# Performance work log

Measured on AMD Instinct MI355X. Metric: run time of the kernel, lower is better.

Reference implementation:

```python
import jax, jax.numpy as jnp
import numpy as np

OUT_DIM = 4096
IN_DIM = 4096
N_NNZ = 1600000
BATCH = 8192


def setup_inputs() -> dict:
    key = jax.random.key(0)
    k1, k2, k3 = jax.random.split(key, 3)
    x = jax.random.normal(k1, (BATCH, IN_DIM), dtype=jnp.float32)
    # COO indices of the transposed kernel: (row=output idx, col=input idx)
    rows = jax.random.randint(k2, (N_NNZ, 1), 0, OUT_DIM, dtype=jnp.int64)
    cols = jax.random.randint(jax.random.fold_in(k2, 1), (N_NNZ, 1), 0, IN_DIM, dtype=jnp.int64)
    indices = jnp.concatenate([rows, cols], axis=1)  # (N_NNZ, 2)
    values = jax.random.normal(k3, (N_NNZ,), dtype=jnp.float32) * 0.02
    return {"x": x, "indices": indices, "values": values}


def reference(x, indices, values):
    # kernel_t is a sparse (OUT_DIM, IN_DIM) matrix. In JAX the efficient
    # faithful form is to scatter the nonzeros into a dense matrix (duplicate
    # indices sum, matching SpMM semantics) and do a single dense GEMM.
    rows = indices[:, 0]
    cols = indices[:, 1]
    W_t = jnp.zeros((OUT_DIM, IN_DIM), dtype=values.dtype).at[rows, cols].add(values)
    # output = (kernel_t @ x^T)^T = x @ kernel_t^T, then ReLU activation.
    out = jax.nn.relu(jnp.einsum("bi,oi->bo", x, W_t))
    return out
```

## Files before the change

### kernel.cpp

```cpp
#include <hip/hip_runtime.h>
#include <hip/hip_bf16.h>
#include <stdint.h>

#define M_DIM 8192
#define N_DIM 4096
#define K_DIM 4096
#define NNZ   1600000

typedef __attribute__((ext_vector_type(8))) short bf16x8;
typedef __attribute__((ext_vector_type(4))) float f32x4;

static const size_t WF32_OFF  = 0;
static const size_t WBF16_OFF = 64ull << 20;
static const size_t XB_OFF    = 96ull << 20;
static const size_t WS_NEED   = 160ull << 20;

__device__ __forceinline__ unsigned short f2bf(float f) {
    union { float f; uint32_t u; } a; a.f = f;
    uint32_t u = a.u;
    uint32_t r = (u + 0x7FFFu + ((u >> 16) & 1u)) >> 16;
    return (unsigned short)r;
}

__global__ void scatter_kernel(const int* __restrict__ idx,
                               const float* __restrict__ vals,
                               float* __restrict__ W) {
    int t = blockIdx.x * blockDim.x + threadIdx.x;
    if (t < NNZ) {
        int2 rc = ((const int2*)idx)[t];
        atomicAdd(&W[(size_t)rc.x * K_DIM + rc.y], vals[t]);
    }
}

__global__ void f32_to_bf16_kernel(const float* __restrict__ src,
                                   unsigned short* __restrict__ dst, int n4) {
    int t = blockIdx.x * blockDim.x + threadIdx.x;
    if (t < n4) {
        float4 v = ((const float4*)src)[t];
        ushort4 o;
        o.x = f2bf(v.x); o.y = f2bf(v.y); o.z = f2bf(v.z); o.w = f2bf(v.w);
        ((ushort4*)dst)[t] = o;
    }
}

#define GLOAD16(gp, lp) __builtin_amdgcn_global_load_lds( \
    (const __attribute__((address_space(1))) void*)(gp),  \
    (__attribute__((address_space(3))) void*)(lp), 16, 0, 0)
#define VMCNT(n)   asm volatile("s_waitcnt vmcnt(" #n ")" ::: "memory")
#define BAR()    __builtin_amdgcn_s_barrier()

#define FRAG(T, r, kk) \
    (*(const bf16x8*)&(T)[(r) * 64 + (((((kk) << 2) + l4) ^ ((r) & 7)) << 3)])

#define STAGE_AG(buf, tt, g) \
    GLOAD16(Ab + (size_t)((g) * 64 + rbase) * K_DIM + (size_t)(tt) * 64 + cs, \
            &sA[buf][(g) * 4096 + wid * 512])
#define STAGE_BG(buf, tt, g) \
    GLOAD16(Bb + (size_t)((g) * 64 + rbase) * K_DIM + (size_t)(tt) * 64 + cs, \
            &sB[buf][(g) * 4096 + wid * 512])

__global__ __launch_bounds__(512, 2) void gemm256_v5(
        const __hip_bfloat16* __restrict__ A,
        const __hip_bfloat16* __restrict__ B,
        float* __restrict__ C)
{
    __shared__ __align__(16) __hip_bfloat16 sA[2][256 * 64];
    __shared__ __align__(16) __hip_bfloat16 sB[2][256 * 64];

    const int tid  = threadIdx.x;
    const int lane = tid & 63;
    const int wid  = tid >> 6;
    const int wr   = wid >> 2;
    const int wc   = wid & 3;
    const int l15  = lane & 15, l4 = lane >> 4;

    const int bid = blockIdx.x;
    const int swz = (bid & 7) * 64 + (bid >> 3);
    const int m0  = (swz >> 4) * 256;
    const int n0  = (swz & 15) * 256;

    const int rbase = tid >> 3;
    const int cs    = ((tid & 7) ^ (rbase & 7)) << 3;

    const __hip_bfloat16* Ab = A + (size_t)m0 * K_DIM;
    const __hip_bfloat16* Bb = B + (size_t)n0 * K_DIM;

    f32x4 acc[8][4] = {};

    STAGE_AG(0, 0, 0); STAGE_AG(0, 0, 1); STAGE_AG(0, 0, 2); STAGE_AG(0, 0, 3);
    STAGE_BG(0, 0, 0); STAGE_BG(0, 0, 1); STAGE_BG(0, 0, 2); STAGE_BG(0, 0, 3);
    STAGE_AG(1, 1, 0); STAGE_AG(1, 1, 1); STAGE_AG(1, 1, 2); STAGE_AG(1, 1, 3);
    STAGE_BG(1, 1, 0); STAGE_BG(1, 1, 1);
    VMCNT(6);
    BAR();

    const int NT = K_DIM / 64;
    #pragma unroll 2
    for (int t = 0; t < NT; ++t) {
        const int c = t & 1;
        const __hip_bfloat16* TA = sA[c];
        const __hip_bfloat16* TB = sB[c];

        bf16x8 aLo[4][2], aHi[4][2], bLo[2][2], bHi[2][2];

        #pragma unroll
        for (int m = 0; m < 4; ++m) {
            const int r = wr * 128 + m * 16 + l15;
            aLo[m][0] = FRAG(TA, r, 0);
            aLo[m][1] = FRAG(TA, r, 1);
        }
        #pragma unroll
        for (int n = 0; n < 2; ++n) {
            const int r = wc * 64 + n * 16 + l15;
            bLo[n][0] = FRAG(TB, r, 0);
            bLo[n][1] = FRAG(TB, r, 1);
        }
        BAR();
        __builtin_amdgcn_s_setprio(1);
        #pragma unroll
        for (int k = 0; k < 2; ++k)
            #pragma unroll
            for (int m = 0; m < 4; ++m)
                #pragma unroll
                for (int n = 0; n < 2; ++n)
                    acc[m][n] = __builtin_amdgcn_mfma_f32_16x16x32_bf16(
                                    aLo[m][k], bLo[n][k], acc[m][n], 0, 0, 0);
        __builtin_amdgcn_s_setprio(0);
        if (t + 1 < NT) { STAGE_BG(c ^ 1, t + 1, 2); STAGE_BG(c ^ 1, t + 1, 3); }

        #pragma unroll
        for (int m = 0; m < 4; ++m) {
            const int r = wr * 128 + 64 + m * 16 + l15;
            aHi[m][0] = FRAG(TA, r, 0);
            aHi[m][1] = FRAG(TA, r, 1);
        }
        BAR();
        __builtin_amdgcn_s_setprio(1);
        #pragma unroll
        for (int k = 0; k < 2; ++k)
            #pragma unroll
            for (int m = 0; m < 4; ++m)
                #pragma unroll
                for (int n = 0; n < 2; ++n)
                    acc[4 + m][n] = __builtin_amdgcn_mfma_f32_16x16x32_bf16(
                                    aHi[m][k], bLo[n][k], acc[4 + m][n], 0, 0, 0);
        __builtin_amdgcn_s_setprio(0);

        #pragma unroll
        for (int n = 0; n < 2; ++n) {
            const int r = wc * 64 + 32 + n * 16 + l15;
            bHi[n][0] = FRAG(TB, r, 0);
            bHi[n][1] = FRAG(TB, r, 1);
        }
        BAR();
        __builtin_amdgcn_s_setprio(1);
        #pragma unroll
        for (int k = 0; k < 2; ++k)
            #pragma unroll
            for (int m = 0; m < 4; ++m)
                #pragma unroll
                for (int n = 0; n < 2; ++n)
                    acc[4 + m][2 + n] = __builtin_amdgcn_mfma_f32_16x16x32_bf16(
                                    aHi[m][k], bHi[n][k], acc[4 + m][2 + n], 0, 0, 0);
        __builtin_amdgcn_s_setprio(0);
        if (t + 2 < NT) {
            STAGE_AG(c, t + 2, 0); STAGE_AG(c, t + 2, 1);
            STAGE_AG(c, t + 2, 2); STAGE_AG(c, t + 2, 3);
        }

        BAR();
        __builtin_amdgcn_s_setprio(1);
        #pragma unroll
        for (int k = 0; k < 2; ++k)
            #pragma unroll
            for (int m = 0; m < 4; ++m)
                #pragma unroll
                for (int n = 0; n < 2; ++n)
                    acc[m][2 + n] = __builtin_amdgcn_mfma_f32_16x16x32_bf16(
                                    aLo[m][k], bHi[n][k], acc[m][2 + n], 0, 0, 0);
        __builtin_amdgcn_s_setprio(0);
        if (t + 2 < NT) { STAGE_BG(c, t + 2, 0); STAGE_BG(c, t + 2, 1); }

        if (t < NT - 2) {
            VMCNT(6);
            BAR();
        } else if (t == NT - 2) {
            VMCNT(0);
            BAR();
        }
    }

    const int row_base = m0 + wr * 128;
    const int col_base = n0 + wc * 64;
    #pragma unroll
    for (int m = 0; m < 8; ++m)
        #pragma unroll
        for (int n = 0; n < 4; ++n) {
            const f32x4 v = acc[m][n];
            const int col = col_base + n * 16 + l15;
            #pragma unroll
            for (int j = 0; j < 4; ++j) {
                const int row = row_base + m * 16 + l4 * 4 + j;
                C[(size_t)row * N_DIM + col] = fmaxf(v[j], 0.0f);
            }
        }
}

__global__ void gemm_f32_fallback(const float* __restrict__ A,
                                  const float* __restrict__ W,
                                  float* __restrict__ C) {
    __shared__ float As[64][17];
    __shared__ float Bs[64][17];
    const int tx = threadIdx.x & 15, ty = threadIdx.x >> 4;
    const int m0 = blockIdx.y * 64, n0 = blockIdx.x * 64;
    float acc[4][4] = {};
    for (int kt = 0; kt < K_DIM; kt += 16) {
        #pragma unroll
        for (int i = 0; i < 4; ++i) {
            int e = threadIdx.x + i * 256;
            int r = e >> 4, k = e & 15;
            As[r][k] = A[(size_t)(m0 + r) * K_DIM + kt + k];
            Bs[r][k] = W[(size_t)(n0 + r) * K_DIM + kt + k];
        }
        __syncthreads();
        #pragma unroll
        for (int k = 0; k < 16; ++k) {
            float av[4], bv[4];
            #pragma unroll
            for (int i = 0; i < 4; ++i) av[i] = As[ty * 4 + i][k];
            #pragma unroll
            for (int i = 0; i < 4; ++i) bv[i] = Bs[tx * 4 + i][k];
            #pragma unroll
            for (int i = 0; i < 4; ++i)
                #pragma unroll
                for (int j = 0; j < 4; ++j) acc[i][j] += av[i] * bv[j];
        }
        __syncthreads();
    }
    #pragma unroll
    for (int i = 0; i < 4; ++i)
        #pragma unroll
        for (int j = 0; j < 4; ++j)
            C[(size_t)(m0 + ty * 4 + i) * N_DIM + n0 + tx * 4 + j] =
                fmaxf(acc[i][j], 0.0f);
}

extern "C" void kernel_launch(void* const* d_in, const int* in_sizes, int n_in,
                              void* d_out, int out_size, void* d_ws, size_t ws_size,
                              hipStream_t stream) {
    const float* x       = (const float*)d_in[0];
    const int*   indices = (const int*)d_in[1];
    const float* values  = (const float*)d_in[2];
    float*       out     = (float*)d_out;

    float* Wf = (float*)((char*)d_ws + WF32_OFF);

    hipMemsetAsync(Wf, 0, (size_t)N_DIM * K_DIM * sizeof(float), stream);
    scatter_kernel<<<(NNZ + 255) / 256, 256, 0, stream>>>(indices, values, Wf);

    if (ws_size >= WS_NEED) {
        unsigned short* Wb = (unsigned short*)((char*)d_ws + WBF16_OFF);
        unsigned short* xb = (unsigned short*)((char*)d_ws + XB_OFF);

        {
            int n4 = (N_DIM * K_DIM) / 4;
            f32_to_bf16_kernel<<<(n4 + 255) / 256, 256, 0, stream>>>(Wf, Wb, n4);
        }
        {
            int n4 = (M_DIM * K_DIM) / 4;
            f32_to_bf16_kernel<<<(n4 + 255) / 256, 256, 0, stream>>>(x, xb, n4);
        }

        gemm256_v5<<<(M_DIM / 256) * (N_DIM / 256), 512, 0, stream>>>(
            (const __hip_bfloat16*)xb, (const __hip_bfloat16*)Wb, out);
    } else {
        gemm_f32_fallback<<<dim3(N_DIM / 64, M_DIM / 64), 256, 0, stream>>>(
            x, Wf, out);
    }
}
```

Measured before the change: 362.3 us.

## Switch GEMM inner loop from 16x16x32 to 32x32x16 bf16 MFMA tiles

Rewrites the 256x256 bf16 GEMM's compute phases to use 32x32x16 MFMA instructions, with 4x2 accumulators of 16 floats per wave instead of 8x4 of 4. Fragment loading and the LDS swizzle are adapted to 32-lane row groups, and the K-step is split into two halves across four phases. Larger MFMA tiles need fewer LDS fragment reads per flop and fewer instructions. The trade-off is a different barrier and staging schedule and a less coalesced epilogue store pattern.

```diff
diff --git a/kernel.cpp b/kernel.cpp
--- a/kernel.cpp
+++ b/kernel.cpp
@@ -8,7 +8,7 @@
 #define NNZ   1600000
 
 typedef __attribute__((ext_vector_type(8))) short bf16x8;
-typedef __attribute__((ext_vector_type(4))) float f32x4;
+typedef __attribute__((ext_vector_type(16))) float f32x16;
 
 static const size_t WF32_OFF  = 0;
 static const size_t WBF16_OFF = 64ull << 20;
@@ -49,8 +49,8 @@
 #define VMCNT(n)   asm volatile("s_waitcnt vmcnt(" #n ")" ::: "memory")
 #define BAR()    __builtin_amdgcn_s_barrier()
 
-#define FRAG(T, r, kk) \
-    (*(const bf16x8*)&(T)[(r) * 64 + (((((kk) << 2) + l4) ^ ((r) & 7)) << 3)])
+#define FRAG32(T, r, kk) \
+    (*(const bf16x8*)&(T)[(r) * 64 + (((((kk) << 1) + l32) ^ ((r) & 7)) << 3)])
 
 #define STAGE_AG(buf, tt, g) \
     GLOAD16(Ab + (size_t)((g) * 64 + rbase) * K_DIM + (size_t)(tt) * 64 + cs, \
@@ -59,7 +59,7 @@
     GLOAD16(Bb + (size_t)((g) * 64 + rbase) * K_DIM + (size_t)(tt) * 64 + cs, \
             &sB[buf][(g) * 4096 + wid * 512])
 
-__global__ __launch_bounds__(512, 2) void gemm256_v5(
+__global__ __launch_bounds__(512, 2) void gemm256_v6(
         const __hip_bfloat16* __restrict__ A,
         const __hip_bfloat16* __restrict__ B,
         float* __restrict__ C)
@@ -72,7 +72,7 @@
     const int wid  = tid >> 6;
     const int wr   = wid >> 2;
     const int wc   = wid & 3;
-    const int l15  = lane & 15, l4 = lane >> 4;
+    const int l31  = lane & 31, l32 = lane >> 5;
 
     const int bid = blockIdx.x;
     const int swz = (bid & 7) * 64 + (bid >> 3);
@@ -85,7 +85,7 @@
     const __hip_bfloat16* Ab = A + (size_t)m0 * K_DIM;
     const __hip_bfloat16* Bb = B + (size_t)n0 * K_DIM;
 
-    f32x4 acc[8][4] = {};
+    f32x16 acc[4][2] = {};
 
     STAGE_AG(0, 0, 0); STAGE_AG(0, 0, 1); STAGE_AG(0, 0, 2); STAGE_AG(0, 0, 3);
     STAGE_BG(0, 0, 0); STAGE_BG(0, 0, 1); STAGE_BG(0, 0, 2); STAGE_BG(0, 0, 3);
@@ -101,85 +101,92 @@
         const __hip_bfloat16* TA = sA[c];
         const __hip_bfloat16* TB = sB[c];
 
-        bf16x8 aLo[4][2], aHi[4][2], bLo[2][2], bHi[2][2];
-
-        #pragma unroll
-        for (int m = 0; m < 4; ++m) {
-            const int r = wr * 128 + m * 16 + l15;
-            aLo[m][0] = FRAG(TA, r, 0);
-            aLo[m][1] = FRAG(TA, r, 1);
-        }
-        #pragma unroll
-        for (int n = 0; n < 2; ++n) {
-            const int r = wc * 64 + n * 16 + l15;
-            bLo[n][0] = FRAG(TB, r, 0);
-            bLo[n][1] = FRAG(TB, r, 1);
-        }
-        BAR();
-        __builtin_amdgcn_s_setprio(1);
-        #pragma unroll
-        for (int k = 0; k < 2; ++k)
-            #pragma unroll
-            for (int m = 0; m < 4; ++m)
-                #pragma unroll
-                for (int n = 0; n < 2; ++n)
-                    acc[m][n] = __builtin_amdgcn_mfma_f32_16x16x32_bf16(
-                                    aLo[m][k], bLo[n][k], acc[m][n], 0, 0, 0);
+        bf16x8 a01[2][2], a23[2][2], b01[2][2], b23[2][2];
+        bf16x8 c01[2][2], c23[2][2];
+
+        #pragma unroll
+        for (int m = 0; m < 2; ++m)
+            #pragma unroll
+            for (int k = 0; k < 2; ++k)
+                a01[m][k] = FRAG32(TA, wr * 128 + m * 32 + l31, k);
+        #pragma unroll
+        for (int n = 0; n < 2; ++n)
+            #pragma unroll
+            for (int k = 0; k < 2; ++k)
+                b01[n][k] = FRAG32(TB, wc * 64 + n * 32 + l31, k);
+        BAR();
+        __builtin_amdgcn_s_setprio(1);
+        #pragma unroll
+        for (int k = 0; k < 2; ++k)
+            #pragma unroll
+            for (int m = 0; m < 2; ++m)
+                #pragma unroll
+                for (int n = 0; n < 2; ++n)
+                    acc[m][n] = __builtin_amdgcn_mfma_f32_32x32x16_bf16(
+                                    a01[m][k], b01[n][k], acc[m][n], 0, 0, 0);
         __builtin_amdgcn_s_setprio(0);
         if (t + 1 < NT) { STAGE_BG(c ^ 1, t + 1, 2); STAGE_BG(c ^ 1, t + 1, 3); }
 
         #pragma unroll
-        for (int m = 0; m < 4; ++m) {
-            const int r = wr * 128 + 64 + m * 16 + l15;
-            aHi[m][0] = FRAG(TA, r, 0);
-            aHi[m][1] = FRAG(TA, r, 1);
-        }
-        BAR();
-        __builtin_amdgcn_s_setprio(1);
-        #pragma unroll
-        for (int k = 0; k < 2; ++k)
-            #pragma unroll
-            for (int m = 0; m < 4; ++m)
-                #pragma unroll
-                for (int n = 0; n < 2; ++n)
-                    acc[4 + m][n] = __builtin_amdgcn_mfma_f32_16x16x32_bf16(
-                                    aHi[m][k], bLo[n][k], acc[4 + m][n], 0, 0, 0);
-        __builtin_amdgcn_s_setprio(0);
-
-        #pragma unroll
-        for (int n = 0; n < 2; ++n) {
-            const int r = wc * 64 + 32 + n * 16 + l15;
-            bHi[n][0] = FRAG(TB, r, 0);
-            bHi[n][1] = FRAG(TB, r, 1);
-        }
-        BAR();
-        __builtin_amdgcn_s_setprio(1);
-        #pragma unroll
-        for (int k = 0; k < 2; ++k)
-            #pragma unroll
-            for (int m = 0; m < 4; ++m)
-                #pragma unroll
-                for (int n = 0; n < 2; ++n)
-                    acc[4 + m][2 + n] = __builtin_amdgcn_mfma_f32_16x16x32_bf16(
-                                    aHi[m][k], bHi[n][k], acc[4 + m][2 + n], 0, 0, 0);
+        for (int m = 0; m < 2; ++m)
+            #pragma unroll
+            for (int k = 0; k < 2; ++k)
+                a23[m][k] = FRAG32(TA, wr * 128 + 64 + m * 32 + l31, k);
+        BAR();
+        __builtin_amdgcn_s_setprio(1);
+        #pragma unroll
+        for (int k = 0; k < 2; ++k)
+            #pragma unroll
+            for (int m = 0; m < 2; ++m)
+                #pragma unroll
+                for (int n = 0; n < 2; ++n)
+                    acc[2 + m][n] = __builtin_amdgcn_mfma_f32_32x32x16_bf16(
+                                    a23[m][k], b01[n][k], acc[2 + m][n], 0, 0, 0);
+        __builtin_amdgcn_s_setprio(0);
+
+        #pragma unroll
+        for (int m = 0; m < 2; ++m)
+            #pragma unroll
+            for (int k = 0; k < 2; ++k)
+                c01[m][k] = FRAG32(TA, wr * 128 + m * 32 + l31, 2 + k);
+        #pragma unroll
+        for (int n = 0; n < 2; ++n)
+            #pragma unroll
+            for (int k = 0; k < 2; ++k)
+                b23[n][k] = FRAG32(TB, wc * 64 + n * 32 + l31, 2 + k);
+        BAR();
+        __builtin_amdgcn_s_setprio(1);
+        #pragma unroll
+        for (int k = 0; k < 2; ++k)
+            #pragma unroll
+            for (int m = 0; m < 2; ++m)
+                #pragma unroll
+                for (int n = 0; n < 2; ++n)
+                    acc[m][n] = __builtin_amdgcn_mfma_f32_32x32x16_bf16(
+                                    c01[m][k], b23[n][k], acc[m][n], 0, 0, 0);
+        __builtin_amdgcn_s_setprio(0);
+        if (t + 2 < NT) { STAGE_BG(c, t + 2, 0); STAGE_BG(c, t + 2, 1); }
+
+        #pragma unroll
+        for (int m = 0; m < 2; ++m)
+            #pragma unroll
+            for (int k = 0; k < 2; ++k)
+                c23[m][k] = FRAG32(TA, wr * 128 + 64 + m * 32 + l31, 2 + k);
+        BAR();
+        __builtin_amdgcn_s_setprio(1);
+        #pragma unroll
+        for (int k = 0; k < 2; ++k)
+            #pragma unroll
+            for (int m = 0; m < 2; ++m)
+                #pragma unroll
+                for (int n = 0; n < 2; ++n)
+                    acc[2 + m][n] = __builtin_amdgcn_mfma_f32_32x32x16_bf16(
+                                    c23[m][k], b23[n][k], acc[2 + m][n], 0, 0, 0);
         __builtin_amdgcn_s_setprio(0);
         if (t + 2 < NT) {
             STAGE_AG(c, t + 2, 0); STAGE_AG(c, t + 2, 1);
             STAGE_AG(c, t + 2, 2); STAGE_AG(c, t + 2, 3);
         }
-
-        BAR();
-        __builtin_amdgcn_s_setprio(1);
-        #pragma unroll
-        for (int k = 0; k < 2; ++k)
-            #pragma unroll
-            for (int m = 0; m < 4; ++m)
-                #pragma unroll
-                for (int n = 0; n < 2; ++n)
-                    acc[m][2 + n] = __builtin_amdgcn_mfma_f32_16x16x32_bf16(
-                                    aLo[m][k], bHi[n][k], acc[m][2 + n], 0, 0, 0);
-        __builtin_amdgcn_s_setprio(0);
-        if (t + 2 < NT) { STAGE_BG(c, t + 2, 0); STAGE_BG(c, t + 2, 1); }
 
         if (t < NT - 2) {
             VMCNT(6);
@@ -193,15 +200,16 @@
     const int row_base = m0 + wr * 128;
     const int col_base = n0 + wc * 64;
     #pragma unroll
-    for (int m = 0; m < 8; ++m)
-        #pragma unroll
-        for (int n = 0; n < 4; ++n) {
-            const f32x4 v = acc[m][n];
-            const int col = col_base + n * 16 + l15;
-            #pragma unroll
-            for (int j = 0; j < 4; ++j) {
-                const int row = row_base + m * 16 + l4 * 4 + j;
-                C[(size_t)row * N_DIM + col] = fmaxf(v[j], 0.0f);
+    for (int mi = 0; mi < 4; ++mi)
+        #pragma unroll
+        for (int ni = 0; ni < 2; ++ni) {
+            const f32x16 v = acc[mi][ni];
+            const int col = col_base + ni * 32 + l31;
+            #pragma unroll
+            for (int reg = 0; reg < 16; ++reg) {
+                const int row = row_base + mi * 32 +
+                                (reg & 3) + ((reg >> 2) << 3) + (l32 << 2);
+                C[(size_t)row * N_DIM + col] = fmaxf(v[reg], 0.0f);
             }
         }
 }
@@ -271,7 +279,7 @@
             f32_to_bf16_kernel<<<(n4 + 255) / 256, 256, 0, stream>>>(x, xb, n4);
         }
 
-        gemm256_v5<<<(M_DIM / 256) * (N_DIM / 256), 512, 0, stream>>>(
+        gemm256_v6<<<(M_DIM / 256) * (N_DIM / 256), 512, 0, stream>>>(
             (const __hip_bfloat16*)xb, (const __hip_bfloat16*)Wb, out);
     } else {
         gemm_f32_fallback<<<dim3(N_DIM / 64, M_DIM / 64), 256, 0, stream>>>(
```

Result: slower. 416.8 us (+15.0%).

## Prefetch next tile's low fragments across iterations and reorder MFMA quadrants

Applied to the files above, without the earlier changes.

Restructures the 256x256 GEMM main loop so the next K-tile's aLo/bLo fragments are read from shared memory during the current iteration's last MFMA phase and carried over in registers. The quadrant order is changed, and all four B groups are now staged together at the end of each iteration, which removes the separate end-of-loop wait and barrier. The goal is to hide LDS read latency and cut one barrier per iteration. The cost is extra registers from the double-buffered fragments, which could spill at 2 blocks per CU. There is also a risk of races, because the prefetch relies on a vmcnt wait whose correctness across all waves depends on the following barrier.

```diff
diff --git a/kernel.cpp b/kernel.cpp
--- a/kernel.cpp
+++ b/kernel.cpp
@@ -59,7 +59,17 @@
     GLOAD16(Bb + (size_t)((g) * 64 + rbase) * K_DIM + (size_t)(tt) * 64 + cs, \
             &sB[buf][(g) * 4096 + wid * 512])
 
-__global__ __launch_bounds__(512, 2) void gemm256_v5(
+#define MFMA16(ACC, AF, BF)                                                   \
+    _Pragma("unroll")                                                         \
+    for (int k = 0; k < 2; ++k)                                               \
+        _Pragma("unroll")                                                     \
+        for (int m = 0; m < 4; ++m)                                           \
+            _Pragma("unroll")                                                 \
+            for (int n = 0; n < 2; ++n)                                       \
+                ACC[m][n] = __builtin_amdgcn_mfma_f32_16x16x32_bf16(          \
+                                AF[m][k], BF[n][k], ACC[m][n], 0, 0, 0)
+
+__global__ __launch_bounds__(512, 2) void gemm256_v7(
         const __hip_bfloat16* __restrict__ A,
         const __hip_bfloat16* __restrict__ B,
         float* __restrict__ C)
@@ -90,30 +100,40 @@
     STAGE_AG(0, 0, 0); STAGE_AG(0, 0, 1); STAGE_AG(0, 0, 2); STAGE_AG(0, 0, 3);
     STAGE_BG(0, 0, 0); STAGE_BG(0, 0, 1); STAGE_BG(0, 0, 2); STAGE_BG(0, 0, 3);
     STAGE_AG(1, 1, 0); STAGE_AG(1, 1, 1); STAGE_AG(1, 1, 2); STAGE_AG(1, 1, 3);
-    STAGE_BG(1, 1, 0); STAGE_BG(1, 1, 1);
-    VMCNT(6);
+    STAGE_BG(1, 1, 0); STAGE_BG(1, 1, 1); STAGE_BG(1, 1, 2); STAGE_BG(1, 1, 3);
+    VMCNT(8);
     BAR();
+
+    bf16x8 aLo[4][2], bLo[2][2];
+    #pragma unroll
+    for (int m = 0; m < 4; ++m) {
+        const int r = wr * 128 + m * 16 + l15;
+        aLo[m][0] = FRAG(sA[0], r, 0);
+        aLo[m][1] = FRAG(sA[0], r, 1);
+    }
+    #pragma unroll
+    for (int n = 0; n < 2; ++n) {
+        const int r = wc * 64 + n * 16 + l15;
+        bLo[n][0] = FRAG(sB[0], r, 0);
+        bLo[n][1] = FRAG(sB[0], r, 1);
+    }
 
     const int NT = K_DIM / 64;
     #pragma unroll 2
     for (int t = 0; t < NT; ++t) {
         const int c = t & 1;
-        const __hip_bfloat16* TA = sA[c];
-        const __hip_bfloat16* TB = sB[c];
-
-        bf16x8 aLo[4][2], aHi[4][2], bLo[2][2], bHi[2][2];
-
-        #pragma unroll
-        for (int m = 0; m < 4; ++m) {
-            const int r = wr * 128 + m * 16 + l15;
-            aLo[m][0] = FRAG(TA, r, 0);
-            aLo[m][1] = FRAG(TA, r, 1);
-        }
+        const __hip_bfloat16* TA  = sA[c];
+        const __hip_bfloat16* TB  = sB[c];
+        const __hip_bfloat16* TAn = sA[c ^ 1];
+        const __hip_bfloat16* TBn = sB[c ^ 1];
+
+        bf16x8 aHi[4][2], bHi[2][2], aLoN[4][2], bLoN[2][2];
+
         #pragma unroll
         for (int n = 0; n < 2; ++n) {
-            const int r = wc * 64 + n * 16 + l15;
-            bLo[n][0] = FRAG(TB, r, 0);
-            bLo[n][1] = FRAG(TB, r, 1);
+            const int r = wc * 64 + 32 + n * 16 + l15;
+            bHi[n][0] = FRAG(TB, r, 0);
+            bHi[n][1] = FRAG(TB, r, 1);
         }
         BAR();
         __builtin_amdgcn_s_setprio(1);
@@ -126,7 +146,6 @@
                     acc[m][n] = __builtin_amdgcn_mfma_f32_16x16x32_bf16(
                                     aLo[m][k], bLo[n][k], acc[m][n], 0, 0, 0);
         __builtin_amdgcn_s_setprio(0);
-        if (t + 1 < NT) { STAGE_BG(c ^ 1, t + 1, 2); STAGE_BG(c ^ 1, t + 1, 3); }
 
         #pragma unroll
         for (int m = 0; m < 4; ++m) {
@@ -142,16 +161,10 @@
             for (int m = 0; m < 4; ++m)
                 #pragma unroll
                 for (int n = 0; n < 2; ++n)
-                    acc[4 + m][n] = __builtin_amdgcn_mfma_f32_16x16x32_bf16(
-                                    aHi[m][k], bLo[n][k], acc[4 + m][n], 0, 0, 0);
+                    acc[m][2 + n] = __builtin_amdgcn_mfma_f32_16x16x32_bf16(
+                                    aLo[m][k], bHi[n][k], acc[m][2 + n], 0, 0, 0);
         __builtin_amdgcn_s_setprio(0);
 
-        #pragma unroll
-        for (int n = 0; n < 2; ++n) {
-            const int r = wc * 64 + 32 + n * 16 + l15;
-            bHi[n][0] = FRAG(TB, r, 0);
-            bHi[n][1] = FRAG(TB, r, 1);
-        }
         BAR();
         __builtin_amdgcn_s_setprio(1);
         #pragma unroll
@@ -168,6 +181,21 @@
             STAGE_AG(c, t + 2, 2); STAGE_AG(c, t + 2, 3);
         }
 
+        if (t + 1 < NT) {
+            if (t + 2 < NT) { VMCNT(4); } else { VMCNT(0); }
+            #pragma unroll
+            for (int m = 0; m < 4; ++m) {
+                const int r = wr * 128 + m * 16 + l15;
+                aLoN[m][0] = FRAG(TAn, r, 0);
+                aLoN[m][1] = FRAG(TAn, r, 1);
+            }
+            #pragma unroll
+            for (int n = 0; n < 2; ++n) {
+                const int r = wc * 64 + n * 16 + l15;
+                bLoN[n][0] = FRAG(TBn, r, 0);
+                bLoN[n][1] = FRAG(TBn, r, 1);
+            }
+        }
         BAR();
         __builtin_amdgcn_s_setprio(1);
         #pragma unroll
@@ -176,17 +204,17 @@
             for (int m = 0; m < 4; ++m)
                 #pragma unroll
                 for (int n = 0; n < 2; ++n)
-                    acc[m][2 + n] = __builtin_amdgcn_mfma_f32_16x16x32_bf16(
-                                    aLo[m][k], bHi[n][k], acc[m][2 + n], 0, 0, 0);
+                    acc[4 + m][n] = __builtin_amdgcn_mfma_f32_16x16x32_bf16(
+                                    aHi[m][k], bLo[n][k], acc[4 + m][n], 0, 0, 0);
         __builtin_amdgcn_s_setprio(0);
-        if (t + 2 < NT) { STAGE_BG(c, t + 2, 0); STAGE_BG(c, t + 2, 1); }
-
-        if (t < NT - 2) {
-            VMCNT(6);
-            BAR();
-        } else if (t == NT - 2) {
-            VMCNT(0);
-            BAR();
+        if (t + 2 < NT) { STAGE_BG(c, t + 2, 0); STAGE_BG(c, t + 2, 1);
+                          STAGE_BG(c, t + 2, 2); STAGE_BG(c, t + 2, 3); }
+
+        if (t + 1 < NT) {
+            #pragma unroll
+            for (int m = 0; m < 4; ++m) { aLo[m][0] = aLoN[m][0]; aLo[m][1] = aLoN[m][1]; }
+            #pragma unroll
+            for (int n = 0; n < 2; ++n) { bLo[n][0] = bLoN[n][0]; bLo[n][1] = bLoN[n][1]; }
         }
     }
 
@@ -271,7 +299,7 @@
             f32_to_bf16_kernel<<<(n4 + 255) / 256, 256, 0, stream>>>(x, xb, n4);
         }
 
-        gemm256_v5<<<(M_DIM / 256) * (N_DIM / 256), 512, 0, stream>>>(
+        gemm256_v7<<<(M_DIM / 256) * (N_DIM / 256), 512, 0, stream>>>(
             (const __hip_bfloat16*)xb, (const __hip_bfloat16*)Wb, out);
     } else {
         gemm_f32_fallback<<<dim3(N_DIM / 64, M_DIM / 64), 256, 0, stream>>>(
```

Result: slower. 652.9 us (+80.2%).

## Fuse bf16 conversions into one launch and reschedule GEMM barriers and prefetch

Applied to the files above, without the earlier changes.

The two fp32-to-bf16 conversion kernels for W and x become one kernel over the combined index range, which saves a launch and its tail. In the GEMM main loop, two of the four per-iteration barriers are removed. The next-tile global-to-LDS prefetch of A and B is moved earlier, right after the remaining barriers, so it overlaps more of the MFMA work. The risk is a race: with fewer barriers, the early prefetch into buffer c may overwrite LDS data that other waves are still reading for fragments.

```diff
diff --git a/kernel.cpp b/kernel.cpp
--- a/kernel.cpp
+++ b/kernel.cpp
@@ -32,15 +32,20 @@
     }
 }
 
-__global__ void f32_to_bf16_kernel(const float* __restrict__ src,
-                                   unsigned short* __restrict__ dst, int n4) {
+__global__ void convert_both_kernel(const float* __restrict__ W,
+                                    const float* __restrict__ x,
+                                    unsigned short* __restrict__ Wb,
+                                    unsigned short* __restrict__ xb,
+                                    int n4W, int n4T) {
     int t = blockIdx.x * blockDim.x + threadIdx.x;
-    if (t < n4) {
-        float4 v = ((const float4*)src)[t];
-        ushort4 o;
-        o.x = f2bf(v.x); o.y = f2bf(v.y); o.z = f2bf(v.z); o.w = f2bf(v.w);
-        ((ushort4*)dst)[t] = o;
-    }
+    if (t >= n4T) return;
+    const float* src; unsigned short* dst; int i;
+    if (t < n4W) { src = W; dst = Wb; i = t; }
+    else         { src = x; dst = xb; i = t - n4W; }
+    float4 v = ((const float4*)src)[i];
+    ushort4 o;
+    o.x = f2bf(v.x); o.y = f2bf(v.y); o.z = f2bf(v.z); o.w = f2bf(v.w);
+    ((ushort4*)dst)[i] = o;
 }
 
 #define GLOAD16(gp, lp) __builtin_amdgcn_global_load_lds( \
@@ -59,7 +64,7 @@
     GLOAD16(Bb + (size_t)((g) * 64 + rbase) * K_DIM + (size_t)(tt) * 64 + cs, \
             &sB[buf][(g) * 4096 + wid * 512])
 
-__global__ __launch_bounds__(512, 2) void gemm256_v5(
+__global__ __launch_bounds__(512, 2) void gemm256_v8(
         const __hip_bfloat16* __restrict__ A,
         const __hip_bfloat16* __restrict__ B,
         float* __restrict__ C)
@@ -115,7 +120,6 @@
             bLo[n][0] = FRAG(TB, r, 0);
             bLo[n][1] = FRAG(TB, r, 1);
         }
-        BAR();
         __builtin_amdgcn_s_setprio(1);
         #pragma unroll
         for (int k = 0; k < 2; ++k)
@@ -127,7 +131,6 @@
                                     aLo[m][k], bLo[n][k], acc[m][n], 0, 0, 0);
         __builtin_amdgcn_s_setprio(0);
         if (t + 1 < NT) { STAGE_BG(c ^ 1, t + 1, 2); STAGE_BG(c ^ 1, t + 1, 3); }
-
         #pragma unroll
         for (int m = 0; m < 4; ++m) {
             const int r = wr * 128 + 64 + m * 16 + l15;
@@ -135,6 +138,11 @@
             aHi[m][1] = FRAG(TA, r, 1);
         }
         BAR();
+
+        if (t + 2 < NT) {
+            STAGE_AG(c, t + 2, 0); STAGE_AG(c, t + 2, 1);
+            STAGE_AG(c, t + 2, 2); STAGE_AG(c, t + 2, 3);
+        }
         __builtin_amdgcn_s_setprio(1);
         #pragma unroll
         for (int k = 0; k < 2; ++k)
@@ -145,7 +153,6 @@
                     acc[4 + m][n] = __builtin_amdgcn_mfma_f32_16x16x32_bf16(
                                     aHi[m][k], bLo[n][k], acc[4 + m][n], 0, 0, 0);
         __builtin_amdgcn_s_setprio(0);
-
         #pragma unroll
         for (int n = 0; n < 2; ++n) {
             const int r = wc * 64 + 32 + n * 16 + l15;
@@ -153,6 +160,8 @@
             bHi[n][1] = FRAG(TB, r, 1);
         }
         BAR();
+
+        if (t + 2 < NT) { STAGE_BG(c, t + 2, 0); STAGE_BG(c, t + 2, 1); }
         __builtin_amdgcn_s_setprio(1);
         #pragma unroll
         for (int k = 0; k < 2; ++k)
@@ -162,14 +171,6 @@
                 for (int n = 0; n < 2; ++n)
                     acc[4 + m][2 + n] = __builtin_amdgcn_mfma_f32_16x16x32_bf16(
                                     aHi[m][k], bHi[n][k], acc[4 + m][2 + n], 0, 0, 0);
-        __builtin_amdgcn_s_setprio(0);
-        if (t + 2 < NT) {
-            STAGE_AG(c, t + 2, 0); STAGE_AG(c, t + 2, 1);
-            STAGE_AG(c, t + 2, 2); STAGE_AG(c, t + 2, 3);
-        }
-
-        BAR();
-        __builtin_amdgcn_s_setprio(1);
         #pragma unroll
         for (int k = 0; k < 2; ++k)
             #pragma unroll
@@ -179,7 +180,6 @@
                     acc[m][2 + n] = __builtin_amdgcn_mfma_f32_16x16x32_bf16(
                                     aLo[m][k], bHi[n][k], acc[m][2 + n], 0, 0, 0);
         __builtin_amdgcn_s_setprio(0);
-        if (t + 2 < NT) { STAGE_BG(c, t + 2, 0); STAGE_BG(c, t + 2, 1); }
 
         if (t < NT - 2) {
             VMCNT(6);
@@ -262,16 +262,12 @@
         unsigned short* Wb = (unsigned short*)((char*)d_ws + WBF16_OFF);
         unsigned short* xb = (unsigned short*)((char*)d_ws + XB_OFF);
 
-        {
-            int n4 = (N_DIM * K_DIM) / 4;
-            f32_to_bf16_kernel<<<(n4 + 255) / 256, 256, 0, stream>>>(Wf, Wb, n4);
-        }
-        {
-            int n4 = (M_DIM * K_DIM) / 4;
-            f32_to_bf16_kernel<<<(n4 + 255) / 256, 256, 0, stream>>>(x, xb, n4);
-        }
-
-        gemm256_v5<<<(M_DIM / 256) * (N_DIM / 256), 512, 0, stream>>>(
+        const int n4W = (N_DIM * K_DIM) / 4;
+        const int n4T = n4W + (M_DIM * K_DIM) / 4;
+        convert_both_kernel<<<(n4T + 255) / 256, 256, 0, stream>>>(
+            Wf, x, Wb, xb, n4W, n4T);
+
+        gemm256_v8<<<(M_DIM / 256) * (N_DIM / 256), 512, 0, stream>>>(
             (const __hip_bfloat16*)xb, (const __hip_bfloat16*)Wb, out);
     } else {
         gemm_f32_fallback<<<dim3(N_DIM / 64, M_DIM / 64), 256, 0, stream>>>(
```

Measured after the change: 363.2 us. Within noise of the previous version (+0.3%).
